# Optimization experiments

Hardware: AMD Instinct MI355X
Metric: run time of the kernel (lower is better)

Reference implementation:

```python
import jax, jax.numpy as jnp
import numpy as np

H = 12          # num heads
D = 768         # hidden size
DH = D // H     # head dim = 64
DE = 768        # encoder hidden size


def setup_inputs() -> dict:
    key = jax.random.key(0)
    ks = jax.random.split(key, 10)
    s = 0.02
    return {
        "hidden_states": jax.random.normal(ks[0], (2, 2048, D), dtype=jnp.float32),
        "encoder_hidden_states": jax.random.normal(ks[1], (2, 4096, DE), dtype=jnp.float32),
        "Wq": jax.random.normal(ks[2], (D, D), dtype=jnp.float32) * s,
        "bq": jnp.zeros((D,), dtype=jnp.float32),
        "Wk": jax.random.normal(ks[3], (DE, D), dtype=jnp.float32) * s,
        "bk": jnp.zeros((D,), dtype=jnp.float32),
        "Wv": jax.random.normal(ks[4], (DE, D), dtype=jnp.float32) * s,
        "bv": jnp.zeros((D,), dtype=jnp.float32),
        "Wo": jax.random.normal(ks[5], (D, D), dtype=jnp.float32) * s,
        "bo": jnp.zeros((D,), dtype=jnp.float32),
    }


def _split_heads(x):
    # [B, S, D] -> [B, H, S, DH]
    B, S, _ = x.shape
    return x.reshape(B, S, H, DH).transpose(0, 2, 1, 3)


def reference(hidden_states, encoder_hidden_states, Wq, bq, Wk, bk, Wv, bv, Wo, bo):
    q = _split_heads(hidden_states @ Wq + bq)              # [B,H,Sq,DH]
    k = _split_heads(encoder_hidden_states @ Wk + bk)      # [B,H,Skv,DH]
    v = _split_heads(encoder_hidden_states @ Wv + bv)      # [B,H,Skv,DH]
    scale = 1.0 / jnp.sqrt(jnp.asarray(DH, dtype=q.dtype))
    scores = jnp.einsum("bhqd,bhkd->bhqk", q, k) * scale   # [B,H,Sq,Skv]
    probs = jax.nn.softmax(scores, axis=-1)
    ctx = jnp.einsum("bhqk,bhkd->bhqd", probs, v)          # [B,H,Sq,DH]
    B, _, Sq, _ = ctx.shape
    ctx = ctx.transpose(0, 2, 1, 3).reshape(B, Sq, D)      # [B,Sq,D]
    return ctx @ Wo + bo
```

## Files before the change

### kernel.cpp

```cpp
#include <hip/hip_runtime.h>

typedef __attribute__((ext_vector_type(8))) short bf16x8;
typedef __attribute__((ext_vector_type(4))) float f32x4;
typedef __attribute__((ext_vector_type(8))) unsigned short u16x8;
typedef __attribute__((ext_vector_type(4))) unsigned short u16x4;
typedef __attribute__((ext_vector_type(4))) int i32x4;

static constexpr int Bsz = 2, SQ = 2048, SKV = 4096, Dm = 768, NH = 12, DH = 64;

#define WAITV(N) asm volatile("s_waitcnt vmcnt(" #N ")" ::: "memory")
#define WAITL0() asm volatile("s_waitcnt lgkmcnt(0)" ::: "memory")

static __device__ __forceinline__ unsigned short f2bf(float f) {
  unsigned int u = __float_as_uint(f);
  u += 0x7fff + ((u >> 16) & 1);
  return (unsigned short)(u >> 16);
}

static __device__ __forceinline__ float fexp2(float x) {
#if __has_builtin(__builtin_amdgcn_exp2f)
  return __builtin_amdgcn_exp2f(x);
#else
  float r; asm("v_exp_f32 %0, %1" : "=v"(r) : "v"(x)); return r;
#endif
}

static __device__ __forceinline__ int cvtpk(float lo, float hi) {
  int r; asm("v_cvt_pk_bf16_f32 %0, %1, %2" : "=v"(r) : "v"(lo), "v"(hi));
  return r;
}

__global__ void cvt_kernel(const float* __restrict__ in, unsigned short* __restrict__ out, int n8) {
  int i = blockIdx.x * blockDim.x + threadIdx.x;
  if (i >= n8) return;
  const float4* p = reinterpret_cast<const float4*>(in) + (size_t)i * 2;
  float4 a = p[0], b = p[1];
  u16x8 o;
  o[0] = f2bf(a.x); o[1] = f2bf(a.y); o[2] = f2bf(a.z); o[3] = f2bf(a.w);
  o[4] = f2bf(b.x); o[5] = f2bf(b.y); o[6] = f2bf(b.z); o[7] = f2bf(b.w);
  *(reinterpret_cast<u16x8*>(out) + i) = o;
}

__global__ void wtrans4(const float* __restrict__ Wq, const float* __restrict__ Wk,
                        const float* __restrict__ Wv, const float* __restrict__ Wo,
                        unsigned short* __restrict__ oq, unsigned short* __restrict__ ok,
                        unsigned short* __restrict__ ov, unsigned short* __restrict__ oo) {
  __shared__ float t[32][33];
  const int z = blockIdx.z;
  const float* W = (z == 0) ? Wq : (z == 1) ? Wk : (z == 2) ? Wv : Wo;
  unsigned short* WT = (z == 0) ? oq : (z == 1) ? ok : (z == 2) ? ov : oo;
  int n0 = blockIdx.x * 32, k0 = blockIdx.y * 32;
  int tx = threadIdx.x, ty = threadIdx.y;
  #pragma unroll
  for (int i = 0; i < 4; ++i)
    t[ty * 4 + i][tx] = W[(size_t)(k0 + ty * 4 + i) * Dm + n0 + tx];
  __syncthreads();
  #pragma unroll
  for (int i = 0; i < 4; ++i)
    WT[(size_t)(n0 + ty * 4 + i) * Dm + k0 + tx] = f2bf(t[tx][ty * 4 + i]);
}

__global__ void vtrans(const unsigned short* __restrict__ vb, unsigned short* __restrict__ vtp) {
  __shared__ unsigned short t[64][65];
  const int kt = blockIdx.x, h = blockIdx.y, b = blockIdx.z;
  const int tid = threadIdx.x;
  const int kr = tid >> 2, dc = (tid & 3) * 16;
  const unsigned short* src = vb + ((size_t)(b * SKV + kt * 64 + kr)) * Dm + h * DH + dc;
  u16x8 a0 = *(const u16x8*)src, a1 = *(const u16x8*)(src + 8);
  #pragma unroll
  for (int j = 0; j < 8; ++j) { t[kr][dc + j] = a0[j]; t[kr][dc + 8 + j] = a1[j]; }
  __syncthreads();
  const int d = tid >> 2, p0 = (tid & 3) * 16;
  u16x8 o0, o1;
  #pragma unroll
  for (int j = 0; j < 16; ++j) {
    int pos = p0 + j;
    int pos5 = pos & 31;
    int kv5 = ((pos5 >> 3) & 3) * 4 + ((pos5 >> 2) & 1) * 16 + (pos5 & 3);
    int kv = (pos & 32) | kv5;
    unsigned short v = t[kv][d];
    if (j < 8) o0[j] = v; else o1[j - 8] = v;
  }
  unsigned short* dst = vtp + ((size_t)(b * NH + h) * DH + d) * SKV + kt * 64 + p0;
  *(u16x8*)dst = o0;
  *(u16x8*)(dst + 8) = o1;
}

template <int BM, int BN, bool F32OUT>
static __device__ __forceinline__ void gemm_body(const unsigned short* __restrict__ A,
                                                 const unsigned short* __restrict__ BT,
                                                 const float* __restrict__ bias,
                                                 void* __restrict__ Cout, float scale,
                                                 int row0, int col0,
                                                 unsigned short* As, unsigned short* Bs) {
  const int tid = threadIdx.x;
  const int wave = tid >> 6, lane = tid & 63;
  const int wr = wave >> 1, wc = wave & 1;
  const int lrow = lane & 15, lk8 = (lane >> 4) << 3;
  constexpr int MI = BM / 32, NJ = BN / 32;
  constexpr int AG = BM / 64, BG = BN / 64;
  constexpr int LPS = AG + BG;
  constexpr int KS = Dm / 32;
  f32x4 acc[MI][NJ] = {};

  auto stage = [&](int buf, int k0) {
    #pragma unroll
    for (int j = 0; j < AG; ++j) {
      int e = (tid + j * 256) * 8; int r = e >> 5, c = e & 31;
      __builtin_amdgcn_global_load_lds(
          (const __attribute__((address_space(1))) void*)(A + (size_t)(row0 + r) * Dm + k0 + c),
          (__attribute__((address_space(3))) void*)(As + buf * (BM * 32) + e), 16, 0, 0);
    }
    #pragma unroll
    for (int j = 0; j < BG; ++j) {
      int e = (tid + j * 256) * 8; int r = e >> 5, c = e & 31;
      __builtin_amdgcn_global_load_lds(
          (const __attribute__((address_space(1))) void*)(BT + (size_t)(col0 + r) * Dm + k0 + c),
          (__attribute__((address_space(3))) void*)(Bs + buf * (BN * 32) + e), 16, 0, 0);
    }
  };

  stage(0, 0); stage(1, 32); stage(2, 64);
  int buf = 0;
  for (int ki = 0; ki < KS; ++ki) {
    if (ki + 2 < KS)      { if constexpr (LPS == 4) WAITV(8); else WAITV(6); }
    else if (ki + 1 < KS) { if constexpr (LPS == 4) WAITV(4); else WAITV(3); }
    else                  WAITV(0);
    __builtin_amdgcn_s_barrier();

    bf16x8 a[MI], b[NJ];
    #pragma unroll
    for (int mi = 0; mi < MI; ++mi)
      a[mi] = *(const bf16x8*)&As[buf * (BM * 32) + (wr * (BM / 2) + mi * 16 + lrow) * 32 + lk8];
    #pragma unroll
    for (int nj = 0; nj < NJ; ++nj)
      b[nj] = *(const bf16x8*)&Bs[buf * (BN * 32) + (wc * (BN / 2) + nj * 16 + lrow) * 32 + lk8];

    WAITL0();
    __builtin_amdgcn_s_barrier();
    if (ki + 3 < KS) stage(buf, (ki + 3) * 32);

    #pragma unroll
    for (int mi = 0; mi < MI; ++mi)
      #pragma unroll
      for (int nj = 0; nj < NJ; ++nj)
        acc[mi][nj] = __builtin_amdgcn_mfma_f32_16x16x32_bf16(a[mi], b[nj], acc[mi][nj], 0, 0, 0);
    buf = (buf == 2) ? 0 : buf + 1;
  }

  const int r4 = (lane >> 4) << 2;
  #pragma unroll
  for (int nj = 0; nj < NJ; ++nj) {
    int gcol = col0 + wc * (BN / 2) + nj * 16 + lrow;
    float bb = bias[gcol];
    #pragma unroll
    for (int mi = 0; mi < MI; ++mi) {
      #pragma unroll
      for (int r = 0; r < 4; ++r) {
        int grow = row0 + wr * (BM / 2) + mi * 16 + r4 + r;
        float v = (acc[mi][nj][r] + bb) * scale;
        if constexpr (F32OUT) ((float*)Cout)[(size_t)grow * Dm + gcol] = v;
        else                  ((unsigned short*)Cout)[(size_t)grow * Dm + gcol] = f2bf(v);
      }
    }
  }
}

__global__ __launch_bounds__(256) void qkv_gemm(const unsigned short* __restrict__ hsb,
                                                const unsigned short* __restrict__ ehsb,
                                                const unsigned short* __restrict__ wqt,
                                                const unsigned short* __restrict__ wkt,
                                                const unsigned short* __restrict__ wvt,
                                                const float* __restrict__ bq,
                                                const float* __restrict__ bk,
                                                const float* __restrict__ bv,
                                                unsigned short* __restrict__ qb,
                                                unsigned short* __restrict__ kb,
                                                unsigned short* __restrict__ vb) {
  __shared__ unsigned short As[3 * 128 * 32];
  __shared__ unsigned short Bs[3 * 128 * 32];
  const int tile = blockIdx.y;
  const unsigned short *A, *BT; const float* bias; unsigned short* out;
  float scale; int row0;
  if (tile < 32)      { A = hsb;  BT = wqt; bias = bq; out = qb; scale = 0.18033688f; row0 = tile * 128; }
  else if (tile < 96) { A = ehsb; BT = wkt; bias = bk; out = kb; scale = 1.0f;        row0 = (tile - 32) * 128; }
  else                { A = ehsb; BT = wvt; bias = bv; out = vb; scale = 1.0f;        row0 = (tile - 96) * 128; }
  gemm_body<128, 128, false>(A, BT, bias, out, scale, row0, blockIdx.x * 128, As, Bs);
}

__global__ __launch_bounds__(256) void o_gemm(const unsigned short* __restrict__ A,
                                              const unsigned short* __restrict__ BT,
                                              const float* __restrict__ bias,
                                              float* __restrict__ Cout) {
  __shared__ unsigned short As[3 * 128 * 32];
  __shared__ unsigned short Bs[3 * 64 * 32];
  gemm_body<128, 64, true>(A, BT, bias, Cout, 1.0f, blockIdx.y * 128, blockIdx.x * 64, As, Bs);
}

__global__ __launch_bounds__(256) void attn_kernel(const unsigned short* __restrict__ Q,
                                                   const unsigned short* __restrict__ K,
                                                   const unsigned short* __restrict__ VT,
                                                   unsigned short* __restrict__ Ctx) {
  __shared__ unsigned short Ks[3][64 * 64];
  __shared__ unsigned short Vs[3][64 * 64];
  const int qt = blockIdx.x, h = blockIdx.y, b = blockIdx.z;
  const int tid = threadIdx.x;
  const int wave = tid >> 6, lane = tid & 63;
  const int lrow = lane & 15, lg = lane >> 4, lk8 = lg << 3;
  const size_t qoff = (size_t)b * SQ * Dm + (size_t)h * DH;
  const size_t koff = (size_t)b * SKV * Dm + (size_t)h * DH;
  const size_t voff = (size_t)(b * NH + h) * DH * SKV;

  const int qrow = qt * 64 + wave * 16 + lrow;
  const bf16x8 qa0 = *(const bf16x8*)(Q + qoff + (size_t)qrow * Dm + lk8);
  const bf16x8 qa1 = *(const bf16x8*)(Q + qoff + (size_t)qrow * Dm + 32 + lk8);

  bf16x8 ones;
  #pragma unroll
  for (int j = 0; j < 8; ++j) ones[j] = (short)0x3F80;

  const unsigned short* ksrc[2];
  const unsigned short* vsrc[2];
  int dste[2];
  #pragma unroll
  for (int c = 0; c < 2; ++c) {
    int db = (tid + c * 256) * 16;
    int r = db >> 7, cb = db & 127;
    int sc = (cb ^ ((r & 7) << 4)) >> 1;
    ksrc[c] = K + koff + (size_t)r * Dm + sc;
    vsrc[c] = VT + voff + (size_t)r * SKV + sc;
    dste[c] = db >> 1;
  }

  auto stage = [&](int buf, int kt) {
    #pragma unroll
    for (int c = 0; c < 2; ++c) {
      __builtin_amdgcn_global_load_lds(
          (const __attribute__((address_space(1))) void*)(ksrc[c] + (size_t)kt * 64 * Dm),
          (__attribute__((address_space(3))) void*)(&Ks[buf][dste[c]]), 16, 0, 0);
      __builtin_amdgcn_global_load_lds(
          (const __attribute__((address_space(1))) void*)(vsrc[c] + kt * 64),
          (__attribute__((address_space(3))) void*)(&Vs[buf][dste[c]]), 16, 0, 0);
    }
  };

  f32x4 acc[4] = {};
  f32x4 acc_l = {};
  const int swz = (lrow & 7) << 4;

  stage(0, 0); stage(1, 1); stage(2, 2);
  int buf = 0;
  constexpr int NT = SKV / 64;
  for (int kt = 0; kt < NT; ++kt) {
    if (kt + 2 < NT)      WAITV(8);
    else if (kt + 1 < NT) WAITV(4);
    else                  WAITV(0);
    __builtin_amdgcn_s_barrier();

    f32x4 s[4] = {};
    __builtin_amdgcn_s_setprio(1);
    #pragma unroll
    for (int ks = 0; ks < 2; ++ks)
      #pragma unroll
      for (int nj = 0; nj < 4; ++nj) {
        const int cb = (ks * 64 + lg * 16) ^ swz;
        bf16x8 kf = *(const bf16x8*)((const char*)&Ks[buf][0] + (nj * 16 + lrow) * 128 + cb);
        s[nj] = __builtin_amdgcn_mfma_f32_16x16x32_bf16(kf, ks ? qa1 : qa0, s[nj], 0, 0, 0);
      }
    __builtin_amdgcn_s_setprio(0);

    float e[4][4];
    #pragma unroll
    for (int nj = 0; nj < 4; ++nj)
      #pragma unroll
      for (int r = 0; r < 4; ++r) e[nj][r] = fexp2(s[nj][r]);

    #pragma unroll
    for (int ks = 0; ks < 2; ++ks) {
      i32x4 pw;
      pw[0] = cvtpk(e[2 * ks][0], e[2 * ks][1]);
      pw[1] = cvtpk(e[2 * ks][2], e[2 * ks][3]);
      pw[2] = cvtpk(e[2 * ks + 1][0], e[2 * ks + 1][1]);
      pw[3] = cvtpk(e[2 * ks + 1][2], e[2 * ks + 1][3]);
      bf16x8 pa = __builtin_bit_cast(bf16x8, pw);
      __builtin_amdgcn_s_setprio(1);
      #pragma unroll
      for (int dj = 0; dj < 4; ++dj) {
        const int cb = (ks * 64 + lg * 16) ^ swz;
        bf16x8 vf = *(const bf16x8*)((const char*)&Vs[buf][0] + (dj * 16 + lrow) * 128 + cb);
        acc[dj] = __builtin_amdgcn_mfma_f32_16x16x32_bf16(vf, pa, acc[dj], 0, 0, 0);
      }
      acc_l = __builtin_amdgcn_mfma_f32_16x16x32_bf16(ones, pa, acc_l, 0, 0, 0);
      __builtin_amdgcn_s_setprio(0);
    }

    WAITL0();
    __builtin_amdgcn_s_barrier();
    if (kt + 3 < NT) stage(buf, kt + 3);
    buf = (buf == 2) ? 0 : buf + 1;
  }

  const float linv = 1.0f / acc_l[0];
  #pragma unroll
  for (int dj = 0; dj < 4; ++dj) {
    u16x4 o;
    #pragma unroll
    for (int r = 0; r < 4; ++r) o[r] = f2bf(acc[dj][r] * linv);
    *(u16x4*)(Ctx + qoff + (size_t)qrow * Dm + dj * 16 + (lg << 2)) = o;
  }
}

extern "C" void kernel_launch(void* const* d_in, const int* in_sizes, int n_in,
                              void* d_out, int out_size, void* d_ws, size_t ws_size,
                              hipStream_t stream) {
  const float* hs  = (const float*)d_in[0];
  const float* ehs = (const float*)d_in[1];
  const float* Wq  = (const float*)d_in[2];
  const float* bq  = (const float*)d_in[3];
  const float* Wk  = (const float*)d_in[4];
  const float* bk  = (const float*)d_in[5];
  const float* Wv  = (const float*)d_in[6];
  const float* bv  = (const float*)d_in[7];
  const float* Wo  = (const float*)d_in[8];
  const float* bo  = (const float*)d_in[9];
  float* out = (float*)d_out;

  unsigned short* hsb  = (unsigned short*)d_ws;
  unsigned short* ehsb = hsb  + (size_t)Bsz * SQ * Dm;
  unsigned short* wqt  = ehsb + (size_t)Bsz * SKV * Dm;
  unsigned short* wkt  = wqt + (size_t)Dm * Dm;
  unsigned short* wvt  = wkt + (size_t)Dm * Dm;
  unsigned short* wot  = wvt + (size_t)Dm * Dm;
  unsigned short* qb   = wot + (size_t)Dm * Dm;
  unsigned short* kb   = qb  + (size_t)Bsz * SQ * Dm;
  unsigned short* vb   = kb  + (size_t)Bsz * SKV * Dm;
  unsigned short* ctxb = vb  + (size_t)Bsz * SKV * Dm;
  unsigned short* vtp  = ehsb;

  const int nHS = Bsz * SQ * Dm, nEHS = Bsz * SKV * Dm;
  cvt_kernel<<<(nHS / 8 + 255) / 256, 256, 0, stream>>>(hs, hsb, nHS / 8);
  cvt_kernel<<<(nEHS / 8 + 255) / 256, 256, 0, stream>>>(ehs, ehsb, nEHS / 8);

  wtrans4<<<dim3(24, 24, 4), dim3(32, 8), 0, stream>>>(Wq, Wk, Wv, Wo, wqt, wkt, wvt, wot);

  qkv_gemm<<<dim3(6, 160), 256, 0, stream>>>(hsb, ehsb, wqt, wkt, wvt, bq, bk, bv, qb, kb, vb);

  vtrans<<<dim3(SKV / 64, NH, Bsz), 256, 0, stream>>>(vb, vtp);

  attn_kernel<<<dim3(SQ / 64, NH, Bsz), 256, 0, stream>>>(qb, kb, vtp, ctxb);

  o_gemm<<<dim3(12, 32), 256, 0, stream>>>(ctxb, wot, bo, out);
}
```

Measured before the change: 249.3 us.

## Switch GEMM and attention to double-buffered pipelines and merge conversion kernels

The GEMM and attention kernels go from triple-buffered LDS staging to double buffering, with an unrolled two-step loop and incrementing pointers so per-stage address math disappears. The GEMM epilogue swaps the MFMA operand order so each lane writes four contiguous columns with vector bias loads and vector stores. The two fp32-to-bf16 conversion launches become one kernel. Halving LDS use may let more blocks fit per CU, but the shallower prefetch depth risks exposing more memory latency.

```diff
diff --git a/kernel.cpp b/kernel.cpp
--- a/kernel.cpp
+++ b/kernel.cpp
@@ -30,14 +30,16 @@
   return r;
 }
 
-__global__ void cvt_kernel(const float* __restrict__ in, unsigned short* __restrict__ out, int n8) {
+__global__ void cvt2_kernel(const float* __restrict__ a, const float* __restrict__ b,
+                            unsigned short* __restrict__ out, int n1, int ntot) {
   int i = blockIdx.x * blockDim.x + threadIdx.x;
-  if (i >= n8) return;
-  const float4* p = reinterpret_cast<const float4*>(in) + (size_t)i * 2;
-  float4 a = p[0], b = p[1];
+  if (i >= ntot) return;
+  const float4* p = (i < n1) ? (reinterpret_cast<const float4*>(a) + (size_t)i * 2)
+                             : (reinterpret_cast<const float4*>(b) + (size_t)(i - n1) * 2);
+  float4 x = p[0], y = p[1];
   u16x8 o;
-  o[0] = f2bf(a.x); o[1] = f2bf(a.y); o[2] = f2bf(a.z); o[3] = f2bf(a.w);
-  o[4] = f2bf(b.x); o[5] = f2bf(b.y); o[6] = f2bf(b.z); o[7] = f2bf(b.w);
+  o[0] = f2bf(x.x); o[1] = f2bf(x.y); o[2] = f2bf(x.z); o[3] = f2bf(x.w);
+  o[4] = f2bf(y.x); o[5] = f2bf(y.y); o[6] = f2bf(y.z); o[7] = f2bf(y.w);
   *(reinterpret_cast<u16x8*>(out) + i) = o;
 }
 
@@ -96,38 +98,46 @@
   const int tid = threadIdx.x;
   const int wave = tid >> 6, lane = tid & 63;
   const int wr = wave >> 1, wc = wave & 1;
-  const int lrow = lane & 15, lk8 = (lane >> 4) << 3;
+  const int lrow = lane & 15, lg = lane >> 4, lk8 = lg << 3;
   constexpr int MI = BM / 32, NJ = BN / 32;
-  constexpr int AG = BM / 64, BG = BN / 64;
-  constexpr int LPS = AG + BG;
+  constexpr int AG = BM / 64, BG = BN / 64, LPS = AG + BG;
   constexpr int KS = Dm / 32;
   f32x4 acc[MI][NJ] = {};
 
-  auto stage = [&](int buf, int k0) {
+  const unsigned short* ap[AG]; int ae[AG];
+  const unsigned short* bp[BG]; int be[BG];
+  #pragma unroll
+  for (int j = 0; j < AG; ++j) {
+    int e = (tid + j * 256) * 8; int r = e >> 5, c = e & 31;
+    ap[j] = A + (size_t)(row0 + r) * Dm + c; ae[j] = e;
+  }
+  #pragma unroll
+  for (int j = 0; j < BG; ++j) {
+    int e = (tid + j * 256) * 8; int r = e >> 5, c = e & 31;
+    bp[j] = BT + (size_t)(col0 + r) * Dm + c; be[j] = e;
+  }
+
+  auto stage = [&](int buf) {
     #pragma unroll
     for (int j = 0; j < AG; ++j) {
-      int e = (tid + j * 256) * 8; int r = e >> 5, c = e & 31;
       __builtin_amdgcn_global_load_lds(
-          (const __attribute__((address_space(1))) void*)(A + (size_t)(row0 + r) * Dm + k0 + c),
-          (__attribute__((address_space(3))) void*)(As + buf * (BM * 32) + e), 16, 0, 0);
+          (const __attribute__((address_space(1))) void*)ap[j],
+          (__attribute__((address_space(3))) void*)(As + buf * (BM * 32) + ae[j]), 16, 0, 0);
+      ap[j] += 32;
     }
     #pragma unroll
     for (int j = 0; j < BG; ++j) {
-      int e = (tid + j * 256) * 8; int r = e >> 5, c = e & 31;
       __builtin_amdgcn_global_load_lds(
-          (const __attribute__((address_space(1))) void*)(BT + (size_t)(col0 + r) * Dm + k0 + c),
-          (__attribute__((address_space(3))) void*)(Bs + buf * (BN * 32) + e), 16, 0, 0);
+          (const __attribute__((address_space(1))) void*)bp[j],
+          (__attribute__((address_space(3))) void*)(Bs + buf * (BN * 32) + be[j]), 16, 0, 0);
+      bp[j] += 32;
     }
   };
 
-  stage(0, 0); stage(1, 32); stage(2, 64);
-  int buf = 0;
-  for (int ki = 0; ki < KS; ++ki) {
-    if (ki + 2 < KS)      { if constexpr (LPS == 4) WAITV(8); else WAITV(6); }
-    else if (ki + 1 < KS) { if constexpr (LPS == 4) WAITV(4); else WAITV(3); }
-    else                  WAITV(0);
+  auto step = [&](int buf, bool doStage, bool last) {
+    if (last) { WAITV(0); }
+    else { if constexpr (LPS == 4) { WAITV(4); } else { WAITV(3); } }
     __builtin_amdgcn_s_barrier();
-
     bf16x8 a[MI], b[NJ];
     #pragma unroll
     for (int mi = 0; mi < MI; ++mi)
@@ -135,32 +145,38 @@
     #pragma unroll
     for (int nj = 0; nj < NJ; ++nj)
       b[nj] = *(const bf16x8*)&Bs[buf * (BN * 32) + (wc * (BN / 2) + nj * 16 + lrow) * 32 + lk8];
-
     WAITL0();
     __builtin_amdgcn_s_barrier();
-    if (ki + 3 < KS) stage(buf, (ki + 3) * 32);
-
+    if (doStage) stage(buf);
     #pragma unroll
     for (int mi = 0; mi < MI; ++mi)
       #pragma unroll
       for (int nj = 0; nj < NJ; ++nj)
-        acc[mi][nj] = __builtin_amdgcn_mfma_f32_16x16x32_bf16(a[mi], b[nj], acc[mi][nj], 0, 0, 0);
-    buf = (buf == 2) ? 0 : buf + 1;
-  }
-
-  const int r4 = (lane >> 4) << 2;
-  #pragma unroll
-  for (int nj = 0; nj < NJ; ++nj) {
-    int gcol = col0 + wc * (BN / 2) + nj * 16 + lrow;
-    float bb = bias[gcol];
-    #pragma unroll
-    for (int mi = 0; mi < MI; ++mi) {
-      #pragma unroll
-      for (int r = 0; r < 4; ++r) {
-        int grow = row0 + wr * (BM / 2) + mi * 16 + r4 + r;
-        float v = (acc[mi][nj][r] + bb) * scale;
-        if constexpr (F32OUT) ((float*)Cout)[(size_t)grow * Dm + gcol] = v;
-        else                  ((unsigned short*)Cout)[(size_t)grow * Dm + gcol] = f2bf(v);
+        acc[mi][nj] = __builtin_amdgcn_mfma_f32_16x16x32_bf16(b[nj], a[mi], acc[mi][nj], 0, 0, 0);
+  };
+
+  stage(0); stage(1);
+  for (int ki = 0; ki + 2 < KS; ki += 2) { step(0, true, false); step(1, true, false); }
+  step(0, false, false);
+  step(1, false, true);
+
+  #pragma unroll
+  for (int mi = 0; mi < MI; ++mi) {
+    const int grow = row0 + wr * (BM / 2) + mi * 16 + lrow;
+    #pragma unroll
+    for (int nj = 0; nj < NJ; ++nj) {
+      const int gcolb = col0 + wc * (BN / 2) + nj * 16 + (lg << 2);
+      const f32x4 bb = *(const f32x4*)&bias[gcolb];
+      if constexpr (F32OUT) {
+        f32x4 v;
+        #pragma unroll
+        for (int r = 0; r < 4; ++r) v[r] = (acc[mi][nj][r] + bb[r]) * scale;
+        *(f32x4*)((float*)Cout + (size_t)grow * Dm + gcolb) = v;
+      } else {
+        u16x4 o;
+        #pragma unroll
+        for (int r = 0; r < 4; ++r) o[r] = f2bf((acc[mi][nj][r] + bb[r]) * scale);
+        *(u16x4*)((unsigned short*)Cout + (size_t)grow * Dm + gcolb) = o;
       }
     }
   }
@@ -177,8 +193,8 @@
                                                 unsigned short* __restrict__ qb,
                                                 unsigned short* __restrict__ kb,
                                                 unsigned short* __restrict__ vb) {
-  __shared__ unsigned short As[3 * 128 * 32];
-  __shared__ unsigned short Bs[3 * 128 * 32];
+  __shared__ unsigned short As[2 * 128 * 32];
+  __shared__ unsigned short Bs[2 * 128 * 32];
   const int tile = blockIdx.y;
   const unsigned short *A, *BT; const float* bias; unsigned short* out;
   float scale; int row0;
@@ -192,8 +208,8 @@
                                               const unsigned short* __restrict__ BT,
                                               const float* __restrict__ bias,
                                               float* __restrict__ Cout) {
-  __shared__ unsigned short As[3 * 128 * 32];
-  __shared__ unsigned short Bs[3 * 64 * 32];
+  __shared__ unsigned short As[2 * 128 * 32];
+  __shared__ unsigned short Bs[2 * 64 * 32];
   gemm_body<128, 64, true>(A, BT, bias, Cout, 1.0f, blockIdx.y * 128, blockIdx.x * 64, As, Bs);
 }
 
@@ -201,8 +217,8 @@
                                                    const unsigned short* __restrict__ K,
                                                    const unsigned short* __restrict__ VT,
                                                    unsigned short* __restrict__ Ctx) {
-  __shared__ unsigned short Ks[3][64 * 64];
-  __shared__ unsigned short Vs[3][64 * 64];
+  __shared__ unsigned short Ks[2][64 * 64];
+  __shared__ unsigned short Vs[2][64 * 64];
   const int qt = blockIdx.x, h = blockIdx.y, b = blockIdx.z;
   const int tid = threadIdx.x;
   const int wave = tid >> 6, lane = tid & 63;
@@ -219,42 +235,35 @@
   #pragma unroll
   for (int j = 0; j < 8; ++j) ones[j] = (short)0x3F80;
 
-  const unsigned short* ksrc[2];
-  const unsigned short* vsrc[2];
-  int dste[2];
-  #pragma unroll
-  for (int c = 0; c < 2; ++c) {
-    int db = (tid + c * 256) * 16;
-    int r = db >> 7, cb = db & 127;
-    int sc = (cb ^ ((r & 7) << 4)) >> 1;
-    ksrc[c] = K + koff + (size_t)r * Dm + sc;
-    vsrc[c] = VT + voff + (size_t)r * SKV + sc;
-    dste[c] = db >> 1;
-  }
-
-  auto stage = [&](int buf, int kt) {
-    #pragma unroll
-    for (int c = 0; c < 2; ++c) {
-      __builtin_amdgcn_global_load_lds(
-          (const __attribute__((address_space(1))) void*)(ksrc[c] + (size_t)kt * 64 * Dm),
-          (__attribute__((address_space(3))) void*)(&Ks[buf][dste[c]]), 16, 0, 0);
-      __builtin_amdgcn_global_load_lds(
-          (const __attribute__((address_space(1))) void*)(vsrc[c] + kt * 64),
-          (__attribute__((address_space(3))) void*)(&Vs[buf][dste[c]]), 16, 0, 0);
-    }
+  const unsigned short *kp0, *kp1, *vp0, *vp1;
+  int de0, de1;
+  {
+    int db0 = tid * 16, db1 = (tid + 256) * 16;
+    int r0 = db0 >> 7, cb0 = db0 & 127, r1 = db1 >> 7, cb1 = db1 & 127;
+    int sc0 = (cb0 ^ ((r0 & 7) << 4)) >> 1, sc1 = (cb1 ^ ((r1 & 7) << 4)) >> 1;
+    kp0 = K + koff + (size_t)r0 * Dm + sc0;  kp1 = K + koff + (size_t)r1 * Dm + sc1;
+    vp0 = VT + voff + (size_t)r0 * SKV + sc0; vp1 = VT + voff + (size_t)r1 * SKV + sc1;
+    de0 = db0 >> 1; de1 = db1 >> 1;
+  }
+
+  auto stage = [&](int buf) {
+    __builtin_amdgcn_global_load_lds((const __attribute__((address_space(1))) void*)kp0,
+        (__attribute__((address_space(3))) void*)(&Ks[buf][de0]), 16, 0, 0);
+    __builtin_amdgcn_global_load_lds((const __attribute__((address_space(1))) void*)vp0,
+        (__attribute__((address_space(3))) void*)(&Vs[buf][de0]), 16, 0, 0);
+    __builtin_amdgcn_global_load_lds((const __attribute__((address_space(1))) void*)kp1,
+        (__attribute__((address_space(3))) void*)(&Ks[buf][de1]), 16, 0, 0);
+    __builtin_amdgcn_global_load_lds((const __attribute__((address_space(1))) void*)vp1,
+        (__attribute__((address_space(3))) void*)(&Vs[buf][de1]), 16, 0, 0);
+    kp0 += 64 * Dm; kp1 += 64 * Dm; vp0 += 64; vp1 += 64;
   };
 
   f32x4 acc[4] = {};
   f32x4 acc_l = {};
   const int swz = (lrow & 7) << 4;
 
-  stage(0, 0); stage(1, 1); stage(2, 2);
-  int buf = 0;
-  constexpr int NT = SKV / 64;
-  for (int kt = 0; kt < NT; ++kt) {
-    if (kt + 2 < NT)      WAITV(8);
-    else if (kt + 1 < NT) WAITV(4);
-    else                  WAITV(0);
+  auto tilebody = [&](int buf, bool doStage, bool last) {
+    if (last) { WAITV(0); } else { WAITV(4); }
     __builtin_amdgcn_s_barrier();
 
     f32x4 s[4] = {};
@@ -296,9 +305,14 @@
 
     WAITL0();
     __builtin_amdgcn_s_barrier();
-    if (kt + 3 < NT) stage(buf, kt + 3);
-    buf = (buf == 2) ? 0 : buf + 1;
-  }
+    if (doStage) stage(buf);
+  };
+
+  stage(0); stage(1);
+  constexpr int NT = SKV / 64;
+  for (int t = 0; t + 2 < NT; t += 2) { tilebody(0, true, false); tilebody(1, true, false); }
+  tilebody(0, false, false);
+  tilebody(1, false, true);
 
   const float linv = 1.0f / acc_l[0];
   #pragma unroll
@@ -338,8 +352,8 @@
   unsigned short* vtp  = ehsb;
 
   const int nHS = Bsz * SQ * Dm, nEHS = Bsz * SKV * Dm;
-  cvt_kernel<<<(nHS / 8 + 255) / 256, 256, 0, stream>>>(hs, hsb, nHS / 8);
-  cvt_kernel<<<(nEHS / 8 + 255) / 256, 256, 0, stream>>>(ehs, ehsb, nEHS / 8);
+  const int n1 = nHS / 8, ntot = (nHS + nEHS) / 8;
+  cvt2_kernel<<<(ntot + 255) / 256, 256, 0, stream>>>(hs, ehs, hsb, n1, ntot);
 
   wtrans4<<<dim3(24, 24, 4), dim3(32, 8), 0, stream>>>(Wq, Wk, Wv, Wo, wqt, wkt, wvt, wot);
 
```

Result: no change. 247.8 us (-0.6%).
